# Optimization experiments

Hardware: AMD Instinct MI355X
Metric: run time of the kernel (lower is better)

The kernel has to match this reference:

```python
import jax, jax.numpy as jnp
import numpy as np

GRID_SIZE = 5      # KANLinear default
SPLINE_ORDER = 3   # KANLinear default
N_CONVS = 16
K = 3              # kernel side
P = K * K          # in_features of each KANLinear
G = GRID_SIZE + SPLINE_ORDER  # number of spline coefficients per input


def make_grid():
    # grid_range=[-1,1]: h = 2/grid_size; extended by spline_order on each side
    h = 2.0 / GRID_SIZE
    return jnp.arange(-SPLINE_ORDER, GRID_SIZE + SPLINE_ORDER + 1, dtype=jnp.float32) * h - 1.0  # (12,)


def b_splines(x, grid):
    # Cox-de Boor recursion, faithful to efficient-kan KANLinear.b_splines.
    # x: (N, P) -> bases: (N, P, G). Grid is identical across the P inputs.
    x = x[..., None]  # (N, P, 1)
    bases = ((x >= grid[:-1]) & (x < grid[1:])).astype(x.dtype)  # (N, P, 11)
    for k in range(1, SPLINE_ORDER + 1):
        left = (x - grid[:-(k + 1)]) / (grid[k:-1] - grid[:-(k + 1)]) * bases[..., :-1]
        right = (grid[k + 1:] - x) / (grid[k + 1:] - grid[1:-k]) * bases[..., 1:]
        bases = left + right
    return bases  # (N, P, G)


def setup_inputs() -> dict:
    key = jax.random.key(0)
    ks = jax.random.split(key, 6)
    B, H, W = 32, 256, 256
    x = jax.random.normal(ks[0], (B, 1, H, W), dtype=jnp.float32)
    # Per-conv KANLinear(in=9, out=1) params, stacked over the 16 convs.
    base_w = jax.random.normal(ks[1], (N_CONVS, P), dtype=jnp.float32) / np.sqrt(P).astype(np.float32)
    spline_w = jax.random.normal(ks[2], (N_CONVS, P, G), dtype=jnp.float32) * 0.1
    spline_scaler = jax.random.normal(ks[3], (N_CONVS, P), dtype=jnp.float32) / np.sqrt(P).astype(np.float32)
    # restore: Conv2d(16, 1, 3, padding=1)
    restore_w = jax.random.normal(ks[4], (1, N_CONVS, K, K), dtype=jnp.float32) / np.sqrt(N_CONVS * P).astype(np.float32)
    restore_b = jax.random.normal(ks[5], (1,), dtype=jnp.float32) * 0.01
    return {"x": x, "base_w": base_w, "spline_w": spline_w,
            "spline_scaler": spline_scaler, "restore_w": restore_w, "restore_b": restore_b}


def reference(x, base_w, spline_w, spline_scaler, restore_w, restore_b):
    B, C, H, W = x.shape  # C == 1
    # Unfold 3x3 patches, stride 1, padding 1 -> (B, H, W, 9), row-major kernel order
    xp = jnp.pad(x, ((0, 0), (0, 0), (1, 1), (1, 1)))
    patches = jnp.stack([xp[:, 0, i:i + H, j:j + W] for i in range(K) for j in range(K)], axis=-1)
    flat = patches.reshape(-1, P)  # (N, 9), N = B*H*W
    bases = b_splines(flat, make_grid())  # (N, 9, G) -- shared across all 16 convs
    scaled_spline_w = spline_w * spline_scaler[..., None]  # (16, 9, G)
    # KANLinear: base (SiLU -> linear) + spline (bases -> linear), per conv
    out = jnp.einsum('np,cp->nc', jax.nn.silu(flat), base_w) \
        + jnp.einsum('npg,cpg->nc', bases, scaled_spline_w)  # (N, 16)
    feat = out.reshape(B, H, W, N_CONVS).transpose(0, 3, 1, 2)  # (B, 16, H, W)
    y = jax.lax.conv_general_dilated(feat, restore_w, (1, 1), [(1, 1), (1, 1)],
                                     dimension_numbers=('NCHW', 'OIHW', 'NCHW'))
    return y + restore_b[None, :, None, None]  # (B, 1, H, W)
```

## Files before the change

### kernel.cpp

```cpp
#include <hip/hip_runtime.h>
#include <math.h>

#define IMG 256
#define TS 32
#define EBASE 736

typedef _Float16 half_t;
typedef _Float16 half2_t __attribute__((ext_vector_type(2)));

__device__ __forceinline__ half2_t bc_h2(unsigned int u) {
    union { unsigned int u; half2_t h; } c; c.u = u; return c.h;
}
__device__ __forceinline__ unsigned int bc_u(half2_t h) {
    union { unsigned int u; half2_t h; } c; c.h = h; return c.u;
}

__device__ __forceinline__ float dot2(half2_t a, half2_t b, float c) {
#if __has_builtin(__builtin_amdgcn_fdot2)
    return __builtin_amdgcn_fdot2(a, b, c, false);
#else
    return fmaf((float)a.x, (float)b.x, fmaf((float)a.y, (float)b.y, c));
#endif
}

__global__ __launch_bounds__(1024) void kkan_precompute(
    const float* __restrict__ bw, const float* __restrict__ sw,
    const float* __restrict__ sc, const float* __restrict__ rw,
    float* __restrict__ ws)
{
    __shared__ float sF[729];
    const int tid = threadIdx.x;
    unsigned int* wse = (unsigned int*)ws + EBASE;
    if (tid < 729) {
        const int u = tid / 81, p = (tid / 9) % 9, j = tid % 9;
        float f = 0.f;
        for (int c = 0; c < 16; ++c) {
            const float w = (j < 8) ? sw[(c * 9 + p) * 8 + j] * sc[c * 9 + p]
                                    : bw[c * 9 + p];
            f += rw[c * 9 + u] * w;
        }
        sF[tid] = f;
        ws[tid] = f;
    } else if (tid < 729 + 288) {
        wse[tid - 729] = 0u;
    }
    __syncthreads();
    if (tid < 45) {
        const int j = tid / 5, sy = tid % 5;
        float e[5];
        for (int sx = 0; sx < 5; ++sx) {
            float acc = 0.f;
            for (int uy = 0; uy < 3; ++uy) {
                const int py = sy - uy;
                if (py < 0 || py > 2) continue;
                for (int ux = 0; ux < 3; ++ux) {
                    const int px = sx - ux;
                    if (px < 0 || px > 2) continue;
                    acc += sF[((uy * 3 + ux) * 9 + (py * 3 + px)) * 9 + j];
                }
            }
            e[sx] = acc;
        }
        unsigned int* oe = wse + j * 32 + sy * 3;
        oe[0] = bc_u(half2_t{(half_t)e[0], (half_t)e[1]});
        oe[1] = bc_u(half2_t{(half_t)e[2], (half_t)e[3]});
        oe[2] = bc_u(half2_t{(half_t)e[4], (half_t)0.f});
        unsigned int* oo = wse + j * 32 + 16 + sy * 3;
        oo[0] = bc_u(half2_t{(half_t)0.f, (half_t)e[0]});
        oo[1] = bc_u(half2_t{(half_t)e[1], (half_t)e[2]});
        oo[2] = bc_u(half2_t{(half_t)e[3], (half_t)e[4]});
    }
}

__global__ __launch_bounds__(256, 6) void kkan_main(
    const float* __restrict__ x, const float* __restrict__ ws,
    const float* __restrict__ rb, float* __restrict__ out)
{
    __shared__ __align__(16) half_t s_phi[9][36][40];

    const int tid = threadIdx.x;
    const int gx0 = blockIdx.x * TS, gy0 = blockIdx.y * TS, b = blockIdx.z;

    {
        uint4 z; z.x = 0u; z.y = 0u; z.z = 0u; z.w = 0u;
        uint4* p = (uint4*)s_phi;
        for (int i = tid; i < 1620; i += 256) p[i] = z;
    }
    __syncthreads();

    const float* xb = x + (size_t)b * (IMG * IMG);

    for (int pix = tid; pix < 36 * 36; pix += 256) {
        const int yy = pix / 36, xx = pix % 36;
        const int gy = gy0 - 2 + yy, gx = gx0 - 2 + xx;
        float v = 0.f;
        if ((unsigned)gy < (unsigned)IMG && (unsigned)gx < (unsigned)IMG)
            v = xb[gy * IMG + gx];

        const float sil = v / (1.f + __expf(-v));

        const int cell = (int)floorf((v + 2.2f) * 2.5f);
        if (cell >= 0 && cell <= 10) {
            const float g0 = (float)(cell - 3) * 0.4f - 1.0f;
            const float u = (v - g0) * 2.5f;
            const float um = 1.f - u, u2 = u * u, u3 = u2 * u;
            const float w0 = um * um * um * (1.f / 6.f);
            const float w1 = (3.f * u3 - 6.f * u2 + 4.f) * (1.f / 6.f);
            const float w2 = (-3.f * u3 + 3.f * u2 + 3.f * u + 1.f) * (1.f / 6.f);
            const float w3 = u3 * (1.f / 6.f);
            const int j0 = cell - 3;
            if (j0 >= 0 && j0 < 8)         s_phi[j0][yy][xx]     = (half_t)w0;
            if (j0 + 1 >= 0 && j0 + 1 < 8) s_phi[j0 + 1][yy][xx] = (half_t)w1;
            if (j0 + 2 >= 0 && j0 + 2 < 8) s_phi[j0 + 2][yy][xx] = (half_t)w2;
            if (j0 + 3 >= 0 && j0 + 3 < 8) s_phi[j0 + 3][yy][xx] = (half_t)w3;
        }
        s_phi[8][yy][xx] = (half_t)sil;
    }
    __syncthreads();

    const int ly = tid >> 3;
    const int lx0 = (tid & 7) * 4;

    const uint4* Eg = (const uint4*)((const unsigned int*)ws + EBASE);

    float aA0 = 0.f, aB0 = 0.f, aC0 = 0.f;
    float aA1 = 0.f, aB1 = 0.f, aC1 = 0.f;
    float aA2 = 0.f, aB2 = 0.f, aC2 = 0.f;
    float aA3 = 0.f, aB3 = 0.f, aC3 = 0.f;

    #pragma unroll
    for (int j = 0; j < 9; ++j) {
        unsigned int ej[32];
        #pragma unroll
        for (int q = 0; q < 8; ++q) {
            const uint4 t = Eg[j * 8 + q];
            ej[q * 4 + 0] = t.x; ej[q * 4 + 1] = t.y;
            ej[q * 4 + 2] = t.z; ej[q * 4 + 3] = t.w;
        }
        #pragma unroll
        for (int sy = 0; sy < 5; ++sy) {
            const half2_t ev0 = bc_h2(ej[sy * 3 + 0]);
            const half2_t ev1 = bc_h2(ej[sy * 3 + 1]);
            const half2_t ev2 = bc_h2(ej[sy * 3 + 2]);
            const half2_t od0 = bc_h2(ej[16 + sy * 3 + 0]);
            const half2_t od1 = bc_h2(ej[16 + sy * 3 + 1]);
            const half2_t od2 = bc_h2(ej[16 + sy * 3 + 2]);
            const uint2* pp = (const uint2*)&s_phi[j][ly + sy][lx0];
            const uint2 ph0 = pp[0], ph1 = pp[1];
            const half2_t P0 = bc_h2(ph0.x), P1 = bc_h2(ph0.y);
            const half2_t P2 = bc_h2(ph1.x), P3 = bc_h2(ph1.y);
            aA0 = dot2(P0, ev0, aA0); aB0 = dot2(P1, ev1, aB0); aC0 = dot2(P2, ev2, aC0);
            aA1 = dot2(P0, od0, aA1); aB1 = dot2(P1, od1, aB1); aC1 = dot2(P2, od2, aC1);
            aA2 = dot2(P1, ev0, aA2); aB2 = dot2(P2, ev1, aB2); aC2 = dot2(P3, ev2, aC2);
            aA3 = dot2(P1, od0, aA3); aB3 = dot2(P2, od1, aB3); aC3 = dot2(P3, od2, aC3);
        }
    }

    float a0 = aA0 + aB0 + aC0;
    float a1 = aA1 + aB1 + aC1;
    float a2 = aA2 + aB2 + aC2;
    float a3 = aA3 + aB3 + aC3;

    const int gy  = gy0 + ly;
    const int gxb = gx0 + lx0;
    if (gy < 2 || gy > 253 || gxb < 2 || gxb > 250) {
        #pragma unroll
        for (int i = 0; i < 4; ++i) {
            const int gx = gxb + i;
            float corr = 0.f;
            for (int uy = 0; uy < 3; ++uy) {
                const int qy = gy + uy - 1;
                for (int ux = 0; ux < 3; ++ux) {
                    const int qx = gx + ux - 1;
                    if ((unsigned)qy < (unsigned)IMG && (unsigned)qx < (unsigned)IMG)
                        continue;
                    for (int p = 0; p < 9; ++p) {
                        const int ry = ly + uy + (p / 3);
                        const int rx = lx0 + i + ux + (p % 3);
                        const float* fp = &ws[((uy * 3 + ux) * 9 + p) * 9];
                        for (int jj = 0; jj < 9; ++jj)
                            corr += fp[jj] * (float)s_phi[jj][ry][rx];
                    }
                }
            }
            if (i == 0) a0 -= corr;
            else if (i == 1) a1 -= corr;
            else if (i == 2) a2 -= corr;
            else a3 -= corr;
        }
    }

    const float rbv = rb[0];
    float4 o4; o4.x = a0 + rbv; o4.y = a1 + rbv; o4.z = a2 + rbv; o4.w = a3 + rbv;
    *(float4*)&out[(size_t)b * (IMG * IMG) + gy * IMG + gxb] = o4;
}

extern "C" void kernel_launch(void* const* d_in, const int* in_sizes, int n_in,
                              void* d_out, int out_size, void* d_ws, size_t ws_size,
                              hipStream_t stream) {
    const float* x             = (const float*)d_in[0];
    const float* base_w        = (const float*)d_in[1];
    const float* spline_w      = (const float*)d_in[2];
    const float* spline_scaler = (const float*)d_in[3];
    const float* restore_w     = (const float*)d_in[4];
    const float* restore_b     = (const float*)d_in[5];
    float* out = (float*)d_out;
    float* ws  = (float*)d_ws;

    kkan_precompute<<<dim3(1), dim3(1024), 0, stream>>>(
        base_w, spline_w, spline_scaler, restore_w, ws);

    dim3 grid(IMG / TS, IMG / TS, 32);
    kkan_main<<<grid, dim3(256), 0, stream>>>(x, ws, restore_b, out);
}
```

Baseline: 45.53 us.

## Split basis computation into a separate pass writing fp16 phi planes to workspace

Adds a kernel that computes the 8 B-spline bases and the SiLU term once per pixel with a branchless truncated-power formula and stores 9 fp16 planes in the workspace. The conv kernel then loads these planes into shared memory instead of recomputing bases for each halo pixel, and fills out-of-image positions with the bases of zero. This removes redundant halo computation and divergent per-pixel branching. In exchange it adds about 9*2 bytes per pixel of global write and read traffic plus an extra launch, and falls back to the fused kernel when the workspace is too small.

New measurement: 76.45 us. 67.9% more time.

```diff
diff --git a/kernel.cpp b/kernel.cpp
--- a/kernel.cpp
+++ b/kernel.cpp
@@ -4,6 +4,9 @@
 #define IMG 256
 #define TS 32
 #define EBASE 736
+#define PHI_BASE 1088
+#define NPIX (32 * 256 * 256)
+#define PLANE NPIX
 
 typedef _Float16 half_t;
 typedef _Float16 half2_t __attribute__((ext_vector_type(2)));
@@ -72,49 +75,88 @@
     }
 }
 
-__global__ __launch_bounds__(256, 6) void kkan_main(
-    const float* __restrict__ x, const float* __restrict__ ws,
+__global__ __launch_bounds__(256) void kkan_phi(
+    const float* __restrict__ x, half_t* __restrict__ phi)
+{
+    const int t = blockIdx.x * 256 + threadIdx.x;
+    const float4 xa = ((const float4*)x)[2 * t];
+    const float4 xb = ((const float4*)x)[2 * t + 1];
+    const float v[8] = {xa.x, xa.y, xa.z, xa.w, xb.x, xb.y, xb.z, xb.w};
+    unsigned int ow[9][4];
+    #pragma unroll
+    for (int k = 0; k < 4; ++k) {
+        float ph[2][9];
+        #pragma unroll
+        for (int e = 0; e < 2; ++e) {
+            const float vv = v[2 * k + e];
+            const float u0 = (vv + 2.2f) * 2.5f;
+            float c[12];
+            #pragma unroll
+            for (int m = 0; m < 12; ++m) {
+                const float tt = fmaxf(u0 - (float)m, 0.f);
+                c[m] = tt * tt * tt;
+            }
+            #pragma unroll
+            for (int j = 0; j < 8; ++j)
+                ph[e][j] = (c[j] - 4.f * c[j + 1] + 6.f * c[j + 2]
+                            - 4.f * c[j + 3] + c[j + 4]) * (1.f / 6.f);
+            ph[e][8] = vv / (1.f + __expf(-vv));
+        }
+        #pragma unroll
+        for (int j = 0; j < 9; ++j)
+            ow[j][k] = bc_u(half2_t{(half_t)ph[0][j], (half_t)ph[1][j]});
+    }
+    #pragma unroll
+    for (int j = 0; j < 9; ++j) {
+        uint4 q; q.x = ow[j][0]; q.y = ow[j][1]; q.z = ow[j][2]; q.w = ow[j][3];
+        ((uint4*)(phi + (size_t)j * PLANE))[t] = q;
+    }
+}
+
+__global__ __launch_bounds__(256, 6) void kkan_conv(
+    const half_t* __restrict__ phi, const float* __restrict__ ws,
     const float* __restrict__ rb, float* __restrict__ out)
 {
     __shared__ __align__(16) half_t s_phi[9][36][40];
 
     const int tid = threadIdx.x;
     const int gx0 = blockIdx.x * TS, gy0 = blockIdx.y * TS, b = blockIdx.z;
-
-    {
-        uint4 z; z.x = 0u; z.y = 0u; z.z = 0u; z.w = 0u;
-        uint4* p = (uint4*)s_phi;
-        for (int i = tid; i < 1620; i += 256) p[i] = z;
-    }
-    __syncthreads();
-
-    const float* xb = x + (size_t)b * (IMG * IMG);
-
-    for (int pix = tid; pix < 36 * 36; pix += 256) {
-        const int yy = pix / 36, xx = pix % 36;
-        const int gy = gy0 - 2 + yy, gx = gx0 - 2 + xx;
-        float v = 0.f;
-        if ((unsigned)gy < (unsigned)IMG && (unsigned)gx < (unsigned)IMG)
-            v = xb[gy * IMG + gx];
-
-        const float sil = v / (1.f + __expf(-v));
-
-        const int cell = (int)floorf((v + 2.2f) * 2.5f);
-        if (cell >= 0 && cell <= 10) {
-            const float g0 = (float)(cell - 3) * 0.4f - 1.0f;
-            const float u = (v - g0) * 2.5f;
-            const float um = 1.f - u, u2 = u * u, u3 = u2 * u;
-            const float w0 = um * um * um * (1.f / 6.f);
-            const float w1 = (3.f * u3 - 6.f * u2 + 4.f) * (1.f / 6.f);
-            const float w2 = (-3.f * u3 + 3.f * u2 + 3.f * u + 1.f) * (1.f / 6.f);
-            const float w3 = u3 * (1.f / 6.f);
-            const int j0 = cell - 3;
-            if (j0 >= 0 && j0 < 8)         s_phi[j0][yy][xx]     = (half_t)w0;
-            if (j0 + 1 >= 0 && j0 + 1 < 8) s_phi[j0 + 1][yy][xx] = (half_t)w1;
-            if (j0 + 2 >= 0 && j0 + 2 < 8) s_phi[j0 + 2][yy][xx] = (half_t)w2;
-            if (j0 + 3 >= 0 && j0 + 3 < 8) s_phi[j0 + 3][yy][xx] = (half_t)w3;
-        }
-        s_phi[8][yy][xx] = (half_t)sil;
+    const int bo = b * (IMG * IMG);
+    unsigned int* sphw = (unsigned int*)s_phi;
+
+    const bool interior = (blockIdx.x >= 1 && blockIdx.x <= 6 &&
+                           blockIdx.y >= 1 && blockIdx.y <= 6);
+    if (interior) {
+        for (int idx = tid; idx < 5832; idx += 256) {
+            const int i = idx / 18, c = idx % 18;
+            const int j = i / 36, r = i % 36;
+            const int gy = gy0 - 2 + r, gx = gx0 - 2 + 2 * c;
+            const unsigned int w =
+                *(const unsigned int*)&phi[(size_t)j * PLANE + bo + gy * IMG + gx];
+            sphw[j * 720 + r * 20 + c] = w;
+        }
+    } else {
+        for (int idx = tid; idx < 5832; idx += 256) {
+            const int i = idx / 18, c = idx % 18;
+            const int j = i / 36, r = i % 36;
+            const int gy = gy0 - 2 + r, gx = gx0 - 2 + 2 * c;
+            const bool rin = (unsigned)gy < (unsigned)IMG;
+            unsigned int w;
+            if (rin && gx >= 0 && gx + 1 < IMG) {
+                w = *(const unsigned int*)&phi[(size_t)j * PLANE + bo + gy * IMG + gx];
+            } else {
+                float p0f = 0.f;
+                if (j == 2 || j == 5) p0f = 1.f / 48.f;
+                else if (j == 3 || j == 4) p0f = 23.f / 48.f;
+                const half_t p0h = (half_t)p0f;
+                const half_t h0 = (rin && (unsigned)gx < (unsigned)IMG)
+                    ? phi[(size_t)j * PLANE + bo + gy * IMG + gx] : p0h;
+                const half_t h1 = (rin && (unsigned)(gx + 1) < (unsigned)IMG)
+                    ? phi[(size_t)j * PLANE + bo + gy * IMG + gx + 1] : p0h;
+                w = bc_u(half2_t{h0, h1});
+            }
+            sphw[j * 720 + r * 20 + c] = w;
+        }
     }
     __syncthreads();
 
@@ -133,9 +175,9 @@
         unsigned int ej[32];
         #pragma unroll
         for (int q = 0; q < 8; ++q) {
-            const uint4 t = Eg[j * 8 + q];
-            ej[q * 4 + 0] = t.x; ej[q * 4 + 1] = t.y;
-            ej[q * 4 + 2] = t.z; ej[q * 4 + 3] = t.w;
+            const uint4 t4 = Eg[j * 8 + q];
+            ej[q * 4 + 0] = t4.x; ej[q * 4 + 1] = t4.y;
+            ej[q * 4 + 2] = t4.z; ej[q * 4 + 3] = t4.w;
         }
         #pragma unroll
         for (int sy = 0; sy < 5; ++sy) {
@@ -195,6 +237,128 @@
     *(float4*)&out[(size_t)b * (IMG * IMG) + gy * IMG + gxb] = o4;
 }
 
+__global__ __launch_bounds__(256, 6) void kkan_fused_fb(
+    const float* __restrict__ x, const float* __restrict__ ws,
+    const float* __restrict__ rb, float* __restrict__ out)
+{
+    __shared__ __align__(16) half_t s_phi[9][36][40];
+
+    const int tid = threadIdx.x;
+    const int gx0 = blockIdx.x * TS, gy0 = blockIdx.y * TS, b = blockIdx.z;
+
+    {
+        uint4 z; z.x = 0u; z.y = 0u; z.z = 0u; z.w = 0u;
+        uint4* p = (uint4*)s_phi;
+        for (int i = tid; i < 1620; i += 256) p[i] = z;
+    }
+    __syncthreads();
+
+    const float* xb = x + (size_t)b * (IMG * IMG);
+
+    for (int pix = tid; pix < 36 * 36; pix += 256) {
+        const int yy = pix / 36, xx = pix % 36;
+        const int gy = gy0 - 2 + yy, gx = gx0 - 2 + xx;
+        float v = 0.f;
+        if ((unsigned)gy < (unsigned)IMG && (unsigned)gx < (unsigned)IMG)
+            v = xb[gy * IMG + gx];
+
+        const float sil = v / (1.f + __expf(-v));
+
+        const int cell = (int)floorf((v + 2.2f) * 2.5f);
+        if (cell >= 0 && cell <= 10) {
+            const float g0 = (float)(cell - 3) * 0.4f - 1.0f;
+            const float u = (v - g0) * 2.5f;
+            const float um = 1.f - u, u2 = u * u, u3 = u2 * u;
+            const float w0 = um * um * um * (1.f / 6.f);
+            const float w1 = (3.f * u3 - 6.f * u2 + 4.f) * (1.f / 6.f);
+            const float w2 = (-3.f * u3 + 3.f * u2 + 3.f * u + 1.f) * (1.f / 6.f);
+            const float w3 = u3 * (1.f / 6.f);
+            const int j0 = cell - 3;
+            if (j0 >= 0 && j0 < 8)         s_phi[j0][yy][xx]     = (half_t)w0;
+            if (j0 + 1 >= 0 && j0 + 1 < 8) s_phi[j0 + 1][yy][xx] = (half_t)w1;
+            if (j0 + 2 >= 0 && j0 + 2 < 8) s_phi[j0 + 2][yy][xx] = (half_t)w2;
+            if (j0 + 3 >= 0 && j0 + 3 < 8) s_phi[j0 + 3][yy][xx] = (half_t)w3;
+        }
+        s_phi[8][yy][xx] = (half_t)sil;
+    }
+    __syncthreads();
+
+    const int ly = tid >> 3;
+    const int lx0 = (tid & 7) * 4;
+    const uint4* Eg = (const uint4*)((const unsigned int*)ws + EBASE);
+
+    float aA0 = 0.f, aB0 = 0.f, aC0 = 0.f;
+    float aA1 = 0.f, aB1 = 0.f, aC1 = 0.f;
+    float aA2 = 0.f, aB2 = 0.f, aC2 = 0.f;
+    float aA3 = 0.f, aB3 = 0.f, aC3 = 0.f;
+
+    #pragma unroll
+    for (int j = 0; j < 9; ++j) {
+        unsigned int ej[32];
+        #pragma unroll
+        for (int q = 0; q < 8; ++q) {
+            const uint4 t4 = Eg[j * 8 + q];
+            ej[q * 4 + 0] = t4.x; ej[q * 4 + 1] = t4.y;
+            ej[q * 4 + 2] = t4.z; ej[q * 4 + 3] = t4.w;
+        }
+        #pragma unroll
+        for (int sy = 0; sy < 5; ++sy) {
+            const half2_t ev0 = bc_h2(ej[sy * 3 + 0]);
+            const half2_t ev1 = bc_h2(ej[sy * 3 + 1]);
+            const half2_t ev2 = bc_h2(ej[sy * 3 + 2]);
+            const half2_t od0 = bc_h2(ej[16 + sy * 3 + 0]);
+            const half2_t od1 = bc_h2(ej[16 + sy * 3 + 1]);
+            const half2_t od2 = bc_h2(ej[16 + sy * 3 + 2]);
+            const uint2* pp = (const uint2*)&s_phi[j][ly + sy][lx0];
+            const uint2 ph0 = pp[0], ph1 = pp[1];
+            const half2_t P0 = bc_h2(ph0.x), P1 = bc_h2(ph0.y);
+            const half2_t P2 = bc_h2(ph1.x), P3 = bc_h2(ph1.y);
+            aA0 = dot2(P0, ev0, aA0); aB0 = dot2(P1, ev1, aB0); aC0 = dot2(P2, ev2, aC0);
+            aA1 = dot2(P0, od0, aA1); aB1 = dot2(P1, od1, aB1); aC1 = dot2(P2, od2, aC1);
+            aA2 = dot2(P1, ev0, aA2); aB2 = dot2(P2, ev1, aB2); aC2 = dot2(P3, ev2, aC2);
+            aA3 = dot2(P1, od0, aA3); aB3 = dot2(P2, od1, aB3); aC3 = dot2(P3, od2, aC3);
+        }
+    }
+
+    float a0 = aA0 + aB0 + aC0;
+    float a1 = aA1 + aB1 + aC1;
+    float a2 = aA2 + aB2 + aC2;
+    float a3 = aA3 + aB3 + aC3;
+
+    const int gy  = gy0 + ly;
+    const int gxb = gx0 + lx0;
+    if (gy < 2 || gy > 253 || gxb < 2 || gxb > 250) {
+        #pragma unroll
+        for (int i = 0; i < 4; ++i) {
+            const int gx = gxb + i;
+            float corr = 0.f;
+            for (int uy = 0; uy < 3; ++uy) {
+                const int qy = gy + uy - 1;
+                for (int ux = 0; ux < 3; ++ux) {
+                    const int qx = gx + ux - 1;
+                    if ((unsigned)qy < (unsigned)IMG && (unsigned)qx < (unsigned)IMG)
+                        continue;
+                    for (int p = 0; p < 9; ++p) {
+                        const int ry = ly + uy + (p / 3);
+                        const int rx = lx0 + i + ux + (p % 3);
+                        const float* fp = &ws[((uy * 3 + ux) * 9 + p) * 9];
+                        for (int jj = 0; jj < 9; ++jj)
+                            corr += fp[jj] * (float)s_phi[jj][ry][rx];
+                    }
+                }
+            }
+            if (i == 0) a0 -= corr;
+            else if (i == 1) a1 -= corr;
+            else if (i == 2) a2 -= corr;
+            else a3 -= corr;
+        }
+    }
+
+    const float rbv = rb[0];
+    float4 o4; o4.x = a0 + rbv; o4.y = a1 + rbv; o4.z = a2 + rbv; o4.w = a3 + rbv;
+    *(float4*)&out[(size_t)b * (IMG * IMG) + gy * IMG + gxb] = o4;
+}
+
 extern "C" void kernel_launch(void* const* d_in, const int* in_sizes, int n_in,
                               void* d_out, int out_size, void* d_ws, size_t ws_size,
                               hipStream_t stream) {
@@ -210,6 +374,12 @@
     kkan_precompute<<<dim3(1), dim3(1024), 0, stream>>>(
         base_w, spline_w, spline_scaler, restore_w, ws);
 
-    dim3 grid(IMG / TS, IMG / TS, 32);
-    kkan_main<<<grid, dim3(256), 0, stream>>>(x, ws, restore_b, out);
-}
+    const size_t need = (size_t)PHI_BASE * 4 + (size_t)9 * PLANE * 2;
+    if (ws_size >= need) {
+        half_t* phi = (half_t*)((char*)d_ws + (size_t)PHI_BASE * 4);
+        kkan_phi<<<dim3(NPIX / 2048), dim3(256), 0, stream>>>(x, phi);
+        kkan_conv<<<dim3(8, 8, 32), dim3(256), 0, stream>>>(phi, ws, restore_b, out);
+    } else {
+        kkan_fused_fb<<<dim3(8, 8, 32), dim3(256), 0, stream>>>(x, ws, restore_b, out);
+    }
+}
```
